# Performance work log

Measured on AMD Instinct MI355X. Metric: run time of the kernel, lower is better.

Reference implementation:

```python
import jax, jax.numpy as jnp
import numpy as np

N = 50000
E = 800000
F_IN = 256
HID = 96
N_CLS = 32
NEG_SLOPE = 0.2


def setup_inputs() -> dict:
    key = jax.random.key(0)
    ks = jax.random.split(key, 10)
    x = jax.random.normal(ks[0], (N, F_IN), dtype=jnp.float32)
    edge_index = jax.random.randint(ks[1], (2, E), 0, N, dtype=jnp.int64)
    s1 = 1.0 / np.sqrt(F_IN)
    s2 = 1.0 / np.sqrt(HID)
    return {
        "x": x,
        "edge_index": edge_index,
        "W1": jax.random.normal(ks[2], (F_IN, HID), dtype=jnp.float32) * s1,
        "a1_src": jax.random.normal(ks[3], (HID,), dtype=jnp.float32) * s2,
        "a1_dst": jax.random.normal(ks[4], (HID,), dtype=jnp.float32) * s2,
        "b1": jnp.zeros((HID,), dtype=jnp.float32),
        "W2": jax.random.normal(ks[5], (HID, N_CLS), dtype=jnp.float32) * s2,
        "a2_src": jax.random.normal(ks[6], (N_CLS,), dtype=jnp.float32) * (1.0 / np.sqrt(N_CLS)),
        "a2_dst": jax.random.normal(ks[7], (N_CLS,), dtype=jnp.float32) * (1.0 / np.sqrt(N_CLS)),
        "b2": jnp.zeros((N_CLS,), dtype=jnp.float32),
    }


def _gat_conv(x, src, dst, W, a_src, a_dst, b, n_nodes):
    # single-head GATConv (PyG defaults), self-loops already in src/dst
    h = x @ W                                  # [N, out]
    alpha_src = h @ a_src                      # [N]
    alpha_dst = h @ a_dst                      # [N]
    e = alpha_src[src] + alpha_dst[dst]        # [E'] edge logits (msg j->i: dst groups)
    e = jnp.where(e > 0, e, NEG_SLOPE * e)     # leaky_relu
    # segment softmax over edges grouped by destination node
    m = jax.ops.segment_max(e, dst, num_segments=n_nodes)
    ex = jnp.exp(e - m[dst])
    denom = jax.ops.segment_sum(ex, dst, num_segments=n_nodes)
    alpha = ex / denom[dst]                    # [E']
    out = jax.ops.segment_sum(alpha[:, None] * h[src], dst, num_segments=n_nodes)
    return out + b


def reference(x, edge_index, W1, a1_src, a1_dst, b1, W2, a2_src, a2_dst, b2):
    loops = jnp.arange(N, dtype=edge_index.dtype)
    src = jnp.concatenate([edge_index[0], loops])
    dst = jnp.concatenate([edge_index[1], loops])
    h = _gat_conv(x, src, dst, W1, a1_src, a1_dst, b1, N)
    h = jax.nn.elu(h)
    # dropout omitted (eval mode, training=False)
    out = _gat_conv(h, src, dst, W2, a2_src, a2_dst, b2, N)
    return jax.nn.log_softmax(out, axis=1)
```

## Files before the change

### kernel.cpp

```cpp
#include <hip/hip_runtime.h>
#include <cstdint>
#include <cstddef>

#define NNODES 50000
#define NEDGES 800000
#define MEDGES (NEDGES + NNODES)
#define FIN    256
#define HID    96
#define NCLS   32
#define NEG_SLOPE 0.2f

#define NBUCK  391
#define BCAP   3072

typedef unsigned int uint32;
typedef __attribute__((ext_vector_type(8))) short short8;
typedef __attribute__((ext_vector_type(4))) float f32x4;

__device__ __forceinline__ ushort bf_round(float f) {
    uint32 u = __float_as_uint(f);
    u += 0x7FFFu + ((u >> 16) & 1u);
    return (ushort)(u >> 16);
}
__device__ __forceinline__ uint32 pack_bf16x2(float a, float b) {
    return (uint32)bf_round(a) | ((uint32)bf_round(b) << 16);
}
__device__ __forceinline__ float bf_lo(uint32 u) { return __uint_as_float(u << 16); }
__device__ __forceinline__ float bf_hi(uint32 u) { return __uint_as_float(u & 0xFFFF0000u); }
__device__ __forceinline__ float lrelu(float t) { return (t > 0.f) ? t : NEG_SLOPE * t; }
__device__ __forceinline__ float af(int i) { return __int_as_float(i); }
__device__ __forceinline__ float elu_fast(float t) { return (t > 0.f) ? t : (__expf(t) - 1.f); }


__global__ __launch_bounds__(256) void packw_kernel(const float* __restrict__ W1,
                                                    ushort* __restrict__ W1p,
                                                    int* __restrict__ gcount) {
    int stride = gridDim.x * 256;
    for (int idx = blockIdx.x * 256 + threadIdx.x; idx < NBUCK; idx += stride)
        gcount[idx] = 0;
    for (int idx = blockIdx.x * 256 + threadIdx.x; idx < 6 * 8 * 64 * 8; idx += stride) {
        int j     = idx & 7;
        int lane  = (idx >> 3) & 63;
        int kstep = (idx >> 9) & 7;
        int ntile = idx >> 12;
        int k = kstep * 32 + ((lane >> 4) << 3) + j;
        int n = ntile * 16 + (lane & 15);
        W1p[idx] = bf_round(W1[(size_t)k * 96 + n]);
    }
}


__global__ __launch_bounds__(256) void bucket1_kernel(const int* __restrict__ ei,
                                                      int* __restrict__ gcount,
                                                      int* __restrict__ staging) {
    __shared__ int hist[NBUCK];
    __shared__ int base_sh[NBUCK];
    for (int i = threadIdx.x; i < NBUCK; i += 256) hist[i] = 0;
    __syncthreads();

    int v[8], rk[8], bk[8];
    int e0 = blockIdx.x * 2048;
#pragma unroll
    for (int i = 0; i < 8; ++i) {
        int e = e0 + i * 256 + threadIdx.x;
        if (e < MEDGES) {
            int s, d;
            if (e < NEDGES) { s = ei[e]; d = ei[NEDGES + e]; }
            else            { s = e - NEDGES; d = s; }
            bk[i] = d >> 7;
            v[i]  = s | ((d & 127) << 16);
            rk[i] = atomicAdd(&hist[bk[i]], 1);
        } else bk[i] = -1;
    }
    __syncthreads();
    for (int i = threadIdx.x; i < NBUCK; i += 256) {
        int c = hist[i];
        base_sh[i] = c ? atomicAdd(&gcount[i], c) : 0;
    }
    __syncthreads();
#pragma unroll
    for (int i = 0; i < 8; ++i) {
        if (bk[i] >= 0) {
            int pos = base_sh[bk[i]] + rk[i];
            if (pos < BCAP)
                staging[(size_t)bk[i] * BCAP + pos] = v[i];
        }
    }
}


__global__ __launch_bounds__(256) void b2gemm1_kernel(const int* __restrict__ staging,
                                                      const int* __restrict__ gcount,
                                                      int* __restrict__ rowptr,
                                                      int* __restrict__ esrc,
                                                      const float* __restrict__ x,
                                                      const ushort* __restrict__ W1p,
                                                      const float* __restrict__ a_src,
                                                      const float* __restrict__ a_dst,
                                                      ushort* __restrict__ h1,
                                                      float* __restrict__ as1,
                                                      float* __restrict__ ad1) {
    __shared__ int dcount[128];
    __shared__ int dincl[128];
    __shared__ int dexcl[128];
    __shared__ int fillc[128];
    __shared__ int red_s[256];

    if (blockIdx.x < NBUCK) {
        const int b = blockIdx.x;
        const int t = threadIdx.x;

        int pv = 0;
        for (int idx = t; idx < b; idx += 256) pv += gcount[idx];
        red_s[t] = pv;
        __syncthreads();
        for (int off2 = 128; off2; off2 >>= 1) {
            if (t < off2) red_s[t] += red_s[t + off2];
            __syncthreads();
        }
        const int ebase = red_s[0];
        const int cnt   = gcount[b];
        const int node0 = b << 7;
        const int* st   = staging + (size_t)b * BCAP;

        for (int i = t; i < 128; i += 256) { dcount[i] = 0; fillc[i] = 0; }
        __syncthreads();

        for (int i = t; i < cnt; i += 256)
            atomicAdd(&dcount[st[i] >> 16], 1);
        __syncthreads();

        if (t < 128) dincl[t] = dcount[t];
        __syncthreads();
        for (int off = 1; off < 128; off <<= 1) {
            int val = (t >= off && t < 128) ? dincl[t - off] : 0;
            __syncthreads();
            if (t < 128) dincl[t] += val;
            __syncthreads();
        }
        if (t < 128) {
            int excl = dincl[t] - dcount[t];
            dexcl[t] = excl;
            int node = node0 + t;
            if (node < NNODES) rowptr[node] = ebase + excl;
        }
        if (b == NBUCK - 1 && t == 0) rowptr[NNODES] = MEDGES;
        __syncthreads();

        for (int i = t; i < cnt; i += 256) {
            int v = st[i];
            int dd = v >> 16;
            int r = atomicAdd(&fillc[dd], 1);
            esrc[ebase + dexcl[dd] + r] = v & 0xFFFF;
        }
        return;
    }

    const int tid  = threadIdx.x;
    const int lane = tid & 63;
    const int wv   = tid >> 6;
    const int m    = lane & 15;
    const int quad = lane >> 4;
    const int node0 = (blockIdx.x - NBUCK) * 64;

    int arow = node0 + wv * 16 + m;
    if (arow >= NNODES) arow = NNODES - 1;
    const float* xr = x + (size_t)arow * FIN + quad * 8;

    const short8* Wp = (const short8*)W1p;

    f32x4 acc[6];
#pragma unroll
    for (int t = 0; t < 6; ++t) acc[t] = (f32x4){0.f, 0.f, 0.f, 0.f};

#pragma unroll
    for (int ks = 0; ks < 8; ++ks) {
        float4 v0 = *(const float4*)(xr + ks * 32);
        float4 v1 = *(const float4*)(xr + ks * 32 + 4);
        short8 a;
        a[0] = (short)bf_round(v0.x); a[1] = (short)bf_round(v0.y);
        a[2] = (short)bf_round(v0.z); a[3] = (short)bf_round(v0.w);
        a[4] = (short)bf_round(v1.x); a[5] = (short)bf_round(v1.y);
        a[6] = (short)bf_round(v1.z); a[7] = (short)bf_round(v1.w);
#pragma unroll
        for (int t = 0; t < 6; ++t) {
            short8 b = Wp[(t * 8 + ks) * 64 + lane];
            acc[t] = __builtin_amdgcn_mfma_f32_16x16x32_bf16(a, b, acc[t], 0, 0, 0);
        }
    }

    float as_reg[6], ad_reg[6];
#pragma unroll
    for (int t = 0; t < 6; ++t) {
        as_reg[t] = a_src[t * 16 + m];
        ad_reg[t] = a_dst[t * 16 + m];
    }

#pragma unroll
    for (int r = 0; r < 4; ++r) {
        int node = node0 + wv * 16 + quad * 4 + r;
        float ps = 0.f, pd = 0.f;
#pragma unroll
        for (int t = 0; t < 6; ++t) {
            ps += acc[t][r] * as_reg[t];
            pd += acc[t][r] * ad_reg[t];
        }
#pragma unroll
        for (int off = 1; off < 16; off <<= 1) {
            ps += __shfl_xor(ps, off);
            pd += __shfl_xor(pd, off);
        }
        if (node < NNODES) {
            ushort* hp = h1 + (size_t)node * 96 + m;
#pragma unroll
            for (int t = 0; t < 6; ++t) hp[t * 16] = bf_round(acc[t][r]);
            if (m == 0) { as1[node] = ps; ad1[node] = pd; }
        }
    }
}


__global__ __launch_bounds__(256) void agg96g2_kernel(const ushort* __restrict__ h,
                                                      const float* __restrict__ asrc,
                                                      const float* __restrict__ adst,
                                                      const float* __restrict__ bias,
                                                      const int* __restrict__ rowptr,
                                                      const int* __restrict__ esrc,
                                                      const float* __restrict__ W2,
                                                      const float* __restrict__ a2s,
                                                      const float* __restrict__ a2d,
                                                      uint32* __restrict__ h2b,
                                                      float* __restrict__ as2,
                                                      float* __restrict__ ad2) {
    __shared__ int2 sa[4][2][32];
    __shared__ __align__(16) float W2t[32 * 100];
    __shared__ __align__(16) float y_sh[4][2][96];

    for (int idx = threadIdx.x; idx < 96 * 32; idx += 256) {
        int c = idx & 31, k = idx >> 5;
        W2t[c * 100 + k] = W2[idx];
    }
    __syncthreads();

    const int wave = threadIdx.x >> 6;
    const int lane = threadIdx.x & 63;
    const int hf   = lane >> 5;
    const int fl32 = lane & 31;
    const int i = blockIdx.x * 8 + wave * 2 + hf;

    const int start = rowptr[i];
    const int deg   = rowptr[i + 1] - start;
    const float ad  = adst[i];
    const float a2s_v = a2s[fl32];
    const float a2d_v = a2d[fl32];
    const int fl    = (fl32 < 24) ? fl32 : 23;

    float acc0 = 0.f, acc1 = 0.f, acc2 = 0.f, acc3 = 0.f;

    if (deg <= 32) {
        bool valid = fl32 < deg;
        int s_reg = valid ? esrc[start + fl32] : 0;
        float e = valid ? lrelu(asrc[s_reg] + ad) : -1e30f;
        float mx = e;
#pragma unroll
        for (int off = 16; off; off >>= 1) mx = fmaxf(mx, __shfl_xor(mx, off));
        float ex = valid ? __expf(e - mx) : 0.f;
        float sum = ex;
#pragma unroll
        for (int off = 16; off; off >>= 1) sum += __shfl_xor(sum, off);
        sa[wave][hf][fl32] = make_int2(s_reg, __float_as_int(ex / sum));

        const int4* sap = (const int4*)&sa[wave][hf][0];

        for (int eb = 0; eb < deg; eb += 8) {
            int4 qa = sap[(eb >> 1) + 0];
            int4 qb = sap[(eb >> 1) + 1];
            int4 qc = sap[(eb >> 1) + 2];
            int4 qd = sap[(eb >> 1) + 3];
            const uint2* r0 = (const uint2*)(h + (size_t)qa.x * 96);
            const uint2* r1 = (const uint2*)(h + (size_t)qa.z * 96);
            const uint2* r2 = (const uint2*)(h + (size_t)qb.x * 96);
            const uint2* r3 = (const uint2*)(h + (size_t)qb.z * 96);
            const uint2* r4 = (const uint2*)(h + (size_t)qc.x * 96);
            const uint2* r5 = (const uint2*)(h + (size_t)qc.z * 96);
            const uint2* r6 = (const uint2*)(h + (size_t)qd.x * 96);
            const uint2* r7 = (const uint2*)(h + (size_t)qd.z * 96);
            uint2 u0 = r0[fl], u1 = r1[fl], u2 = r2[fl], u3 = r3[fl];
            uint2 u4 = r4[fl], u5 = r5[fl], u6 = r6[fl], u7 = r7[fl];
            float a0 = af(qa.y), a1 = af(qa.w), a2 = af(qb.y), a3 = af(qb.w);
            float a4 = af(qc.y), a5 = af(qc.w), a6 = af(qd.y), a7 = af(qd.w);
            acc0 += a0 * bf_lo(u0.x) + a1 * bf_lo(u1.x) + a2 * bf_lo(u2.x) + a3 * bf_lo(u3.x)
                  + a4 * bf_lo(u4.x) + a5 * bf_lo(u5.x) + a6 * bf_lo(u6.x) + a7 * bf_lo(u7.x);
            acc1 += a0 * bf_hi(u0.x) + a1 * bf_hi(u1.x) + a2 * bf_hi(u2.x) + a3 * bf_hi(u3.x)
                  + a4 * bf_hi(u4.x) + a5 * bf_hi(u5.x) + a6 * bf_hi(u6.x) + a7 * bf_hi(u7.x);
            acc2 += a0 * bf_lo(u0.y) + a1 * bf_lo(u1.y) + a2 * bf_lo(u2.y) + a3 * bf_lo(u3.y)
                  + a4 * bf_lo(u4.y) + a5 * bf_lo(u5.y) + a6 * bf_lo(u6.y) + a7 * bf_lo(u7.y);
            acc3 += a0 * bf_hi(u0.y) + a1 * bf_hi(u1.y) + a2 * bf_hi(u2.y) + a3 * bf_hi(u3.y)
                  + a4 * bf_hi(u4.y) + a5 * bf_hi(u5.y) + a6 * bf_hi(u6.y) + a7 * bf_hi(u7.y);
        }
    } else {
        float mx = -1e30f;
        for (int p = start + fl32; p < start + deg; p += 32)
            mx = fmaxf(mx, lrelu(asrc[esrc[p]] + ad));
#pragma unroll
        for (int off = 16; off; off >>= 1) mx = fmaxf(mx, __shfl_xor(mx, off));
        float sum = 0.f;
        for (int p = start + fl32; p < start + deg; p += 32)
            sum += __expf(lrelu(asrc[esrc[p]] + ad) - mx);
#pragma unroll
        for (int off = 16; off; off >>= 1) sum += __shfl_xor(sum, off);
        float inv = 1.f / sum;
        for (int e = 0; e < deg; ++e) {
            int s = esrc[start + e];
            float a = __expf(lrelu(asrc[s] + ad) - mx) * inv;
            uint2 u = ((const uint2*)(h + (size_t)s * 96))[fl];
            acc0 += a * bf_lo(u.x);
            acc1 += a * bf_hi(u.x);
            acc2 += a * bf_lo(u.y);
            acc3 += a * bf_hi(u.y);
        }
    }

    if (fl32 < 24) {
        float* yp = &y_sh[wave][hf][4 * fl32];
        yp[0] = elu_fast(acc0 + bias[4 * fl32 + 0]);
        yp[1] = elu_fast(acc1 + bias[4 * fl32 + 1]);
        yp[2] = elu_fast(acc2 + bias[4 * fl32 + 2]);
        yp[3] = elu_fast(acc3 + bias[4 * fl32 + 3]);
    }
    asm volatile("s_waitcnt lgkmcnt(0)" ::: "memory");

    const float* yrow = &y_sh[wave][hf][0];
    const float* wcol = W2t + fl32 * 100;
    float h2c = 0.f;
#pragma unroll
    for (int k = 0; k < 96; k += 4) {
        float4 yv = *(const float4*)(yrow + k);
        float4 wv = *(const float4*)(wcol + k);
        h2c = fmaf(yv.x, wv.x, h2c);
        h2c = fmaf(yv.y, wv.y, h2c);
        h2c = fmaf(yv.z, wv.z, h2c);
        h2c = fmaf(yv.w, wv.w, h2c);
    }

    float ps = h2c * a2s_v;
    float pd = h2c * a2d_v;
#pragma unroll
    for (int off = 1; off < 32; off <<= 1) {
        ps += __shfl_xor(ps, off);
        pd += __shfl_xor(pd, off);
    }
    float partner = __shfl_xor(h2c, 16);
    if (fl32 < 16)
        h2b[(size_t)i * 16 + fl32] = pack_bf16x2(h2c, partner);
    if (fl32 == 0) { as2[i] = ps; ad2[i] = pd; }
}


__global__ __launch_bounds__(256) void agg32_kernel(const uint32* __restrict__ h2b,
                                                    const float* __restrict__ asrc,
                                                    const float* __restrict__ adst,
                                                    const float* __restrict__ bias,
                                                    const int* __restrict__ rowptr,
                                                    const int* __restrict__ esrc,
                                                    float* __restrict__ out) {
    __shared__ int2 sa[4][2][32];
    const int wave = threadIdx.x >> 6;
    const int lane = threadIdx.x & 63;
    const int hf   = lane >> 5;
    const int fl32 = lane & 31;
    const int i = blockIdx.x * 8 + wave * 2 + hf;

    const int start = rowptr[i];
    const int deg   = rowptr[i + 1] - start;
    const float ad  = adst[i];
    const int g  = fl32 >> 3;
    const int fl = fl32 & 7;

    float acc[4];
#pragma unroll
    for (int j = 0; j < 4; ++j) acc[j] = 0.f;

    if (deg <= 32) {
        bool valid = fl32 < deg;
        int s_reg = valid ? esrc[start + fl32] : 0;
        float e = valid ? lrelu(asrc[s_reg] + ad) : -1e30f;
        float mx = e;
#pragma unroll
        for (int off = 16; off; off >>= 1) mx = fmaxf(mx, __shfl_xor(mx, off));
        float ex = valid ? __expf(e - mx) : 0.f;
        float sum = ex;
#pragma unroll
        for (int off = 16; off; off >>= 1) sum += __shfl_xor(sum, off);
        sa[wave][hf][fl32] = make_int2(s_reg, __float_as_int(ex / sum));

#pragma unroll 2
        for (int eb = 0; eb < deg; eb += 4) {
            int e0 = eb + g;
            int2 q = sa[wave][hf][(e0 < 32) ? e0 : 31];
            float a = (e0 < deg) ? af(q.y) : 0.f;
            const uint2* hr = (const uint2*)(h2b + (size_t)q.x * 16);
            uint2 u = hr[fl];
            acc[0] = fmaf(a, bf_lo(u.x), acc[0]);
            acc[1] = fmaf(a, bf_hi(u.x), acc[1]);
            acc[2] = fmaf(a, bf_lo(u.y), acc[2]);
            acc[3] = fmaf(a, bf_hi(u.y), acc[3]);
        }
    } else {
        float mx = -1e30f;
        for (int p = start + fl32; p < start + deg; p += 32)
            mx = fmaxf(mx, lrelu(asrc[esrc[p]] + ad));
#pragma unroll
        for (int off = 16; off; off >>= 1) mx = fmaxf(mx, __shfl_xor(mx, off));
        float sum = 0.f;
        for (int p = start + fl32; p < start + deg; p += 32)
            sum += __expf(lrelu(asrc[esrc[p]] + ad) - mx);
#pragma unroll
        for (int off = 16; off; off >>= 1) sum += __shfl_xor(sum, off);
        float inv = 1.f / sum;
        for (int p = start + g; p < start + deg; p += 4) {
            int s = esrc[p];
            float a = __expf(lrelu(asrc[s] + ad) - mx) * inv;
            const uint2* hr = (const uint2*)(h2b + (size_t)s * 16);
            uint2 u = hr[fl];
            acc[0] = fmaf(a, bf_lo(u.x), acc[0]);
            acc[1] = fmaf(a, bf_hi(u.x), acc[1]);
            acc[2] = fmaf(a, bf_lo(u.y), acc[2]);
            acc[3] = fmaf(a, bf_hi(u.y), acc[3]);
        }
    }

#pragma unroll
    for (int j = 0; j < 4; ++j) {
        acc[j] += __shfl_xor(acc[j], 8);
        acc[j] += __shfl_xor(acc[j], 16);
    }

    float z0 = acc[0] + bias[2 * fl];
    float z1 = acc[1] + bias[2 * fl + 16];
    float z2 = acc[2] + bias[2 * fl + 1];
    float z3 = acc[3] + bias[2 * fl + 17];
    float m2 = fmaxf(fmaxf(z0, z1), fmaxf(z2, z3));
#pragma unroll
    for (int off = 4; off; off >>= 1) m2 = fmaxf(m2, __shfl_xor(m2, off));
    float s2 = __expf(z0 - m2) + __expf(z1 - m2) + __expf(z2 - m2) + __expf(z3 - m2);
#pragma unroll
    for (int off = 4; off; off >>= 1) s2 += __shfl_xor(s2, off);
    float ls = m2 + __logf(s2);
    if (fl32 < 8) {
        float* op = out + (size_t)i * 32;
        op[2 * fl]      = z0 - ls;
        op[2 * fl + 16] = z1 - ls;
        op[2 * fl + 1]  = z2 - ls;
        op[2 * fl + 17] = z3 - ls;
    }
}


extern "C" void kernel_launch(void* const* d_in, const int* in_sizes, int n_in,
                              void* d_out, int out_size, void* d_ws, size_t ws_size,
                              hipStream_t stream) {
    const float* x   = (const float*)d_in[0];
    const int*   ei  = (const int*)d_in[1];
    const float* W1  = (const float*)d_in[2];
    const float* a1s = (const float*)d_in[3];
    const float* a1d = (const float*)d_in[4];
    const float* b1  = (const float*)d_in[5];
    const float* W2  = (const float*)d_in[6];
    const float* a2s = (const float*)d_in[7];
    const float* a2d = (const float*)d_in[8];
    const float* b2  = (const float*)d_in[9];
    float* out = (float*)d_out;

    size_t off = 0;
    auto alloc = [&](size_t bytes) {
        void* p = (char*)d_ws + off;
        off += (bytes + 255) & ~(size_t)255;
        return p;
    };
    ushort* h1    = (ushort*)alloc((size_t)NNODES * HID * 2);
    uint32* h2b   = (uint32*)alloc((size_t)NNODES * 16 * 4);
    int*  staging = (int*)alloc((size_t)NBUCK * BCAP * 4);
    float* as1    = (float*)alloc((size_t)NNODES * 4);
    float* ad1    = (float*)alloc((size_t)NNODES * 4);
    float* as2    = (float*)alloc((size_t)NNODES * 4);
    float* ad2    = (float*)alloc((size_t)NNODES * 4);
    int*   rowptr = (int*)alloc((size_t)(NNODES + 1) * 4);
    int*   esrc   = (int*)alloc((size_t)MEDGES * 4);
    ushort* W1p   = (ushort*)alloc((size_t)6 * 8 * 64 * 8 * 2);
    int*   gcount = (int*)alloc((size_t)NBUCK * 4);

    const int nbB1    = (MEDGES + 2047) / 2048;
    const int nbGemm  = (NNODES + 63) / 64;
    const int nbAggP  = NNODES / 8;

    packw_kernel<<<16, 256, 0, stream>>>(W1, W1p, gcount);
    bucket1_kernel<<<nbB1, 256, 0, stream>>>(ei, gcount, staging);
    b2gemm1_kernel<<<NBUCK + nbGemm, 256, 0, stream>>>(staging, gcount, rowptr, esrc,
                                                       x, W1p, a1s, a1d, h1, as1, ad1);
    agg96g2_kernel<<<nbAggP, 256, 0, stream>>>(h1, as1, ad1, b1, rowptr, esrc,
                                               W2, a2s, a2d, h2b, as2, ad2);
    agg32_kernel<<<nbAggP, 256, 0, stream>>>(h2b, as2, ad2, b2, rowptr, esrc, out);
}
```

Before: 207.4 us.

## Fuse all five GAT stages into one cooperative persistent kernel with grid syncs

Result: slower. 456.7 us (+120.2%).

```diff
diff --git a/kernel.cpp b/kernel.cpp
--- a/kernel.cpp
+++ b/kernel.cpp
@@ -1,6 +1,9 @@
 #include <hip/hip_runtime.h>
+#include <hip/hip_cooperative_groups.h>
 #include <cstdint>
 #include <cstddef>
+
+namespace cg = cooperative_groups;
 
 #define NNODES 50000
 #define NEDGES 800000
@@ -12,6 +15,9 @@
 
 #define NBUCK  391
 #define BCAP   3072
+#define NCHUNK ((MEDGES + 2047) / 2048)
+#define NGEMM1 ((NNODES + 63) / 64)
+#define NAGG   (NNODES / 8)
 
 typedef unsigned int uint32;
 typedef __attribute__((ext_vector_type(8))) short short8;
@@ -31,428 +37,396 @@
 __device__ __forceinline__ float af(int i) { return __int_as_float(i); }
 __device__ __forceinline__ float elu_fast(float t) { return (t > 0.f) ? t : (__expf(t) - 1.f); }
 
-
-__global__ __launch_bounds__(256) void packw_kernel(const float* __restrict__ W1,
-                                                    ushort* __restrict__ W1p,
-                                                    int* __restrict__ gcount) {
-    int stride = gridDim.x * 256;
-    for (int idx = blockIdx.x * 256 + threadIdx.x; idx < NBUCK; idx += stride)
-        gcount[idx] = 0;
-    for (int idx = blockIdx.x * 256 + threadIdx.x; idx < 6 * 8 * 64 * 8; idx += stride) {
-        int j     = idx & 7;
-        int lane  = (idx >> 3) & 63;
-        int kstep = (idx >> 9) & 7;
-        int ntile = idx >> 12;
-        int k = kstep * 32 + ((lane >> 4) << 3) + j;
-        int n = ntile * 16 + (lane & 15);
-        W1p[idx] = bf_round(W1[(size_t)k * 96 + n]);
-    }
-}
-
-
-__global__ __launch_bounds__(256) void bucket1_kernel(const int* __restrict__ ei,
-                                                      int* __restrict__ gcount,
-                                                      int* __restrict__ staging) {
-    __shared__ int hist[NBUCK];
-    __shared__ int base_sh[NBUCK];
-    for (int i = threadIdx.x; i < NBUCK; i += 256) hist[i] = 0;
-    __syncthreads();
-
-    int v[8], rk[8], bk[8];
-    int e0 = blockIdx.x * 2048;
-#pragma unroll
-    for (int i = 0; i < 8; ++i) {
-        int e = e0 + i * 256 + threadIdx.x;
-        if (e < MEDGES) {
-            int s, d;
-            if (e < NEDGES) { s = ei[e]; d = ei[NEDGES + e]; }
-            else            { s = e - NEDGES; d = s; }
-            bk[i] = d >> 7;
-            v[i]  = s | ((d & 127) << 16);
-            rk[i] = atomicAdd(&hist[bk[i]], 1);
-        } else bk[i] = -1;
-    }
-    __syncthreads();
-    for (int i = threadIdx.x; i < NBUCK; i += 256) {
-        int c = hist[i];
-        base_sh[i] = c ? atomicAdd(&gcount[i], c) : 0;
-    }
-    __syncthreads();
-#pragma unroll
-    for (int i = 0; i < 8; ++i) {
-        if (bk[i] >= 0) {
-            int pos = base_sh[bk[i]] + rk[i];
-            if (pos < BCAP)
-                staging[(size_t)bk[i] * BCAP + pos] = v[i];
-        }
-    }
-}
-
-
-__global__ __launch_bounds__(256) void b2gemm1_kernel(const int* __restrict__ staging,
-                                                      const int* __restrict__ gcount,
-                                                      int* __restrict__ rowptr,
-                                                      int* __restrict__ esrc,
-                                                      const float* __restrict__ x,
-                                                      const ushort* __restrict__ W1p,
-                                                      const float* __restrict__ a_src,
-                                                      const float* __restrict__ a_dst,
-                                                      ushort* __restrict__ h1,
-                                                      float* __restrict__ as1,
-                                                      float* __restrict__ ad1) {
-    __shared__ int dcount[128];
-    __shared__ int dincl[128];
-    __shared__ int dexcl[128];
-    __shared__ int fillc[128];
-    __shared__ int red_s[256];
-
-    if (blockIdx.x < NBUCK) {
-        const int b = blockIdx.x;
-        const int t = threadIdx.x;
-
-        int pv = 0;
-        for (int idx = t; idx < b; idx += 256) pv += gcount[idx];
-        red_s[t] = pv;
-        __syncthreads();
-        for (int off2 = 128; off2; off2 >>= 1) {
-            if (t < off2) red_s[t] += red_s[t + off2];
-            __syncthreads();
-        }
-        const int ebase = red_s[0];
-        const int cnt   = gcount[b];
-        const int node0 = b << 7;
-        const int* st   = staging + (size_t)b * BCAP;
-
-        for (int i = t; i < 128; i += 256) { dcount[i] = 0; fillc[i] = 0; }
-        __syncthreads();
-
-        for (int i = t; i < cnt; i += 256)
-            atomicAdd(&dcount[st[i] >> 16], 1);
-        __syncthreads();
-
-        if (t < 128) dincl[t] = dcount[t];
-        __syncthreads();
-        for (int off = 1; off < 128; off <<= 1) {
-            int val = (t >= off && t < 128) ? dincl[t - off] : 0;
-            __syncthreads();
-            if (t < 128) dincl[t] += val;
-            __syncthreads();
-        }
-        if (t < 128) {
-            int excl = dincl[t] - dcount[t];
-            dexcl[t] = excl;
-            int node = node0 + t;
-            if (node < NNODES) rowptr[node] = ebase + excl;
-        }
-        if (b == NBUCK - 1 && t == 0) rowptr[NNODES] = MEDGES;
-        __syncthreads();
-
-        for (int i = t; i < cnt; i += 256) {
-            int v = st[i];
-            int dd = v >> 16;
-            int r = atomicAdd(&fillc[dd], 1);
-            esrc[ebase + dexcl[dd] + r] = v & 0xFFFF;
-        }
-        return;
-    }
-
-    const int tid  = threadIdx.x;
-    const int lane = tid & 63;
-    const int wv   = tid >> 6;
-    const int m    = lane & 15;
-    const int quad = lane >> 4;
-    const int node0 = (blockIdx.x - NBUCK) * 64;
-
-    int arow = node0 + wv * 16 + m;
-    if (arow >= NNODES) arow = NNODES - 1;
-    const float* xr = x + (size_t)arow * FIN + quad * 8;
-
-    const short8* Wp = (const short8*)W1p;
-
-    f32x4 acc[6];
-#pragma unroll
-    for (int t = 0; t < 6; ++t) acc[t] = (f32x4){0.f, 0.f, 0.f, 0.f};
-
-#pragma unroll
-    for (int ks = 0; ks < 8; ++ks) {
-        float4 v0 = *(const float4*)(xr + ks * 32);
-        float4 v1 = *(const float4*)(xr + ks * 32 + 4);
-        short8 a;
-        a[0] = (short)bf_round(v0.x); a[1] = (short)bf_round(v0.y);
-        a[2] = (short)bf_round(v0.z); a[3] = (short)bf_round(v0.w);
-        a[4] = (short)bf_round(v1.x); a[5] = (short)bf_round(v1.y);
-        a[6] = (short)bf_round(v1.z); a[7] = (short)bf_round(v1.w);
-#pragma unroll
-        for (int t = 0; t < 6; ++t) {
-            short8 b = Wp[(t * 8 + ks) * 64 + lane];
-            acc[t] = __builtin_amdgcn_mfma_f32_16x16x32_bf16(a, b, acc[t], 0, 0, 0);
-        }
-    }
-
-    float as_reg[6], ad_reg[6];
-#pragma unroll
-    for (int t = 0; t < 6; ++t) {
-        as_reg[t] = a_src[t * 16 + m];
-        ad_reg[t] = a_dst[t * 16 + m];
-    }
-
-#pragma unroll
-    for (int r = 0; r < 4; ++r) {
-        int node = node0 + wv * 16 + quad * 4 + r;
-        float ps = 0.f, pd = 0.f;
-#pragma unroll
-        for (int t = 0; t < 6; ++t) {
-            ps += acc[t][r] * as_reg[t];
-            pd += acc[t][r] * ad_reg[t];
-        }
-#pragma unroll
-        for (int off = 1; off < 16; off <<= 1) {
-            ps += __shfl_xor(ps, off);
-            pd += __shfl_xor(pd, off);
-        }
-        if (node < NNODES) {
-            ushort* hp = h1 + (size_t)node * 96 + m;
-#pragma unroll
-            for (int t = 0; t < 6; ++t) hp[t * 16] = bf_round(acc[t][r]);
-            if (m == 0) { as1[node] = ps; ad1[node] = pd; }
-        }
-    }
-}
-
-
-__global__ __launch_bounds__(256) void agg96g2_kernel(const ushort* __restrict__ h,
-                                                      const float* __restrict__ asrc,
-                                                      const float* __restrict__ adst,
-                                                      const float* __restrict__ bias,
-                                                      const int* __restrict__ rowptr,
-                                                      const int* __restrict__ esrc,
-                                                      const float* __restrict__ W2,
-                                                      const float* __restrict__ a2s,
-                                                      const float* __restrict__ a2d,
-                                                      uint32* __restrict__ h2b,
-                                                      float* __restrict__ as2,
-                                                      float* __restrict__ ad2) {
-    __shared__ int2 sa[4][2][32];
-    __shared__ __align__(16) float W2t[32 * 100];
-    __shared__ __align__(16) float y_sh[4][2][96];
-
-    for (int idx = threadIdx.x; idx < 96 * 32; idx += 256) {
-        int c = idx & 31, k = idx >> 5;
-        W2t[c * 100 + k] = W2[idx];
-    }
-    __syncthreads();
-
-    const int wave = threadIdx.x >> 6;
-    const int lane = threadIdx.x & 63;
+struct __align__(16) SU {
+    union {
+        struct { int hist[NBUCK]; int base_sh[NBUCK]; } s1;
+        struct { int dcount[128]; int dincl[128]; int dexcl[128];
+                 int fillc[128]; int red_s[256]; } s2;
+        struct { int2 sa[4][2][32]; float W2n[96 * 32]; float y_sh[4][2][96]; } s3;
+        struct { int2 sa[4][2][32]; } s4;
+    } u;
+};
+
+
+__global__ __launch_bounds__(256) void fused_all(
+        const float* __restrict__ x,   const int* __restrict__ ei,
+        const float* __restrict__ W1,
+        const float* __restrict__ a1s, const float* __restrict__ a1d,
+        const float* __restrict__ b1,
+        const float* __restrict__ W2,
+        const float* __restrict__ a2s, const float* __restrict__ a2d,
+        const float* __restrict__ b2,
+        float* __restrict__ out,
+        ushort* __restrict__ h1, uint32* __restrict__ h2b,
+        int* __restrict__ staging, float* __restrict__ as1, float* __restrict__ ad1,
+        float* __restrict__ as2, float* __restrict__ ad2,
+        int* __restrict__ rowptr, int* __restrict__ esrc,
+        ushort* __restrict__ W1p, int* __restrict__ gcount) {
+    __shared__ SU sh;
+    cg::grid_group grid = cg::this_grid();
+
+    const int t    = threadIdx.x;
+    const int wave = t >> 6;
+    const int lane = t & 63;
     const int hf   = lane >> 5;
     const int fl32 = lane & 31;
-    const int i = blockIdx.x * 8 + wave * 2 + hf;
-
-    const int start = rowptr[i];
-    const int deg   = rowptr[i + 1] - start;
-    const float ad  = adst[i];
-    const float a2s_v = a2s[fl32];
-    const float a2d_v = a2d[fl32];
-    const int fl    = (fl32 < 24) ? fl32 : 23;
-
-    float acc0 = 0.f, acc1 = 0.f, acc2 = 0.f, acc3 = 0.f;
-
-    if (deg <= 32) {
-        bool valid = fl32 < deg;
-        int s_reg = valid ? esrc[start + fl32] : 0;
-        float e = valid ? lrelu(asrc[s_reg] + ad) : -1e30f;
-        float mx = e;
-#pragma unroll
-        for (int off = 16; off; off >>= 1) mx = fmaxf(mx, __shfl_xor(mx, off));
-        float ex = valid ? __expf(e - mx) : 0.f;
-        float sum = ex;
-#pragma unroll
-        for (int off = 16; off; off >>= 1) sum += __shfl_xor(sum, off);
-        sa[wave][hf][fl32] = make_int2(s_reg, __float_as_int(ex / sum));
-
-        const int4* sap = (const int4*)&sa[wave][hf][0];
-
-        for (int eb = 0; eb < deg; eb += 8) {
-            int4 qa = sap[(eb >> 1) + 0];
-            int4 qb = sap[(eb >> 1) + 1];
-            int4 qc = sap[(eb >> 1) + 2];
-            int4 qd = sap[(eb >> 1) + 3];
-            const uint2* r0 = (const uint2*)(h + (size_t)qa.x * 96);
-            const uint2* r1 = (const uint2*)(h + (size_t)qa.z * 96);
-            const uint2* r2 = (const uint2*)(h + (size_t)qb.x * 96);
-            const uint2* r3 = (const uint2*)(h + (size_t)qb.z * 96);
-            const uint2* r4 = (const uint2*)(h + (size_t)qc.x * 96);
-            const uint2* r5 = (const uint2*)(h + (size_t)qc.z * 96);
-            const uint2* r6 = (const uint2*)(h + (size_t)qd.x * 96);
-            const uint2* r7 = (const uint2*)(h + (size_t)qd.z * 96);
-            uint2 u0 = r0[fl], u1 = r1[fl], u2 = r2[fl], u3 = r3[fl];
-            uint2 u4 = r4[fl], u5 = r5[fl], u6 = r6[fl], u7 = r7[fl];
-            float a0 = af(qa.y), a1 = af(qa.w), a2 = af(qb.y), a3 = af(qb.w);
-            float a4 = af(qc.y), a5 = af(qc.w), a6 = af(qd.y), a7 = af(qd.w);
-            acc0 += a0 * bf_lo(u0.x) + a1 * bf_lo(u1.x) + a2 * bf_lo(u2.x) + a3 * bf_lo(u3.x)
-                  + a4 * bf_lo(u4.x) + a5 * bf_lo(u5.x) + a6 * bf_lo(u6.x) + a7 * bf_lo(u7.x);
-            acc1 += a0 * bf_hi(u0.x) + a1 * bf_hi(u1.x) + a2 * bf_hi(u2.x) + a3 * bf_hi(u3.x)
-                  + a4 * bf_hi(u4.x) + a5 * bf_hi(u5.x) + a6 * bf_hi(u6.x) + a7 * bf_hi(u7.x);
-            acc2 += a0 * bf_lo(u0.y) + a1 * bf_lo(u1.y) + a2 * bf_lo(u2.y) + a3 * bf_lo(u3.y)
-                  + a4 * bf_lo(u4.y) + a5 * bf_lo(u5.y) + a6 * bf_lo(u6.y) + a7 * bf_lo(u7.y);
-            acc3 += a0 * bf_hi(u0.y) + a1 * bf_hi(u1.y) + a2 * bf_hi(u2.y) + a3 * bf_hi(u3.y)
-                  + a4 * bf_hi(u4.y) + a5 * bf_hi(u5.y) + a6 * bf_hi(u6.y) + a7 * bf_hi(u7.y);
-        }
-    } else {
-        float mx = -1e30f;
-        for (int p = start + fl32; p < start + deg; p += 32)
-            mx = fmaxf(mx, lrelu(asrc[esrc[p]] + ad));
-#pragma unroll
-        for (int off = 16; off; off >>= 1) mx = fmaxf(mx, __shfl_xor(mx, off));
-        float sum = 0.f;
-        for (int p = start + fl32; p < start + deg; p += 32)
-            sum += __expf(lrelu(asrc[esrc[p]] + ad) - mx);
-#pragma unroll
-        for (int off = 16; off; off >>= 1) sum += __shfl_xor(sum, off);
-        float inv = 1.f / sum;
-        for (int e = 0; e < deg; ++e) {
-            int s = esrc[start + e];
-            float a = __expf(lrelu(asrc[s] + ad) - mx) * inv;
-            uint2 u = ((const uint2*)(h + (size_t)s * 96))[fl];
-            acc0 += a * bf_lo(u.x);
-            acc1 += a * bf_hi(u.x);
-            acc2 += a * bf_lo(u.y);
-            acc3 += a * bf_hi(u.y);
-        }
-    }
-
-    if (fl32 < 24) {
-        float* yp = &y_sh[wave][hf][4 * fl32];
-        yp[0] = elu_fast(acc0 + bias[4 * fl32 + 0]);
-        yp[1] = elu_fast(acc1 + bias[4 * fl32 + 1]);
-        yp[2] = elu_fast(acc2 + bias[4 * fl32 + 2]);
-        yp[3] = elu_fast(acc3 + bias[4 * fl32 + 3]);
-    }
-    asm volatile("s_waitcnt lgkmcnt(0)" ::: "memory");
-
-    const float* yrow = &y_sh[wave][hf][0];
-    const float* wcol = W2t + fl32 * 100;
-    float h2c = 0.f;
-#pragma unroll
-    for (int k = 0; k < 96; k += 4) {
-        float4 yv = *(const float4*)(yrow + k);
-        float4 wv = *(const float4*)(wcol + k);
-        h2c = fmaf(yv.x, wv.x, h2c);
-        h2c = fmaf(yv.y, wv.y, h2c);
-        h2c = fmaf(yv.z, wv.z, h2c);
-        h2c = fmaf(yv.w, wv.w, h2c);
-    }
-
-    float ps = h2c * a2s_v;
-    float pd = h2c * a2d_v;
-#pragma unroll
-    for (int off = 1; off < 32; off <<= 1) {
-        ps += __shfl_xor(ps, off);
-        pd += __shfl_xor(pd, off);
-    }
-    float partner = __shfl_xor(h2c, 16);
-    if (fl32 < 16)
-        h2b[(size_t)i * 16 + fl32] = pack_bf16x2(h2c, partner);
-    if (fl32 == 0) { as2[i] = ps; ad2[i] = pd; }
-}
-
-
-__global__ __launch_bounds__(256) void agg32_kernel(const uint32* __restrict__ h2b,
-                                                    const float* __restrict__ asrc,
-                                                    const float* __restrict__ adst,
-                                                    const float* __restrict__ bias,
-                                                    const int* __restrict__ rowptr,
-                                                    const int* __restrict__ esrc,
-                                                    float* __restrict__ out) {
-    __shared__ int2 sa[4][2][32];
-    const int wave = threadIdx.x >> 6;
-    const int lane = threadIdx.x & 63;
-    const int hf   = lane >> 5;
-    const int fl32 = lane & 31;
-    const int i = blockIdx.x * 8 + wave * 2 + hf;
-
-    const int start = rowptr[i];
-    const int deg   = rowptr[i + 1] - start;
-    const float ad  = adst[i];
-    const int g  = fl32 >> 3;
-    const int fl = fl32 & 7;
-
-    float acc[4];
-#pragma unroll
-    for (int j = 0; j < 4; ++j) acc[j] = 0.f;
-
-    if (deg <= 32) {
-        bool valid = fl32 < deg;
-        int s_reg = valid ? esrc[start + fl32] : 0;
-        float e = valid ? lrelu(asrc[s_reg] + ad) : -1e30f;
-        float mx = e;
-#pragma unroll
-        for (int off = 16; off; off >>= 1) mx = fmaxf(mx, __shfl_xor(mx, off));
-        float ex = valid ? __expf(e - mx) : 0.f;
-        float sum = ex;
-#pragma unroll
-        for (int off = 16; off; off >>= 1) sum += __shfl_xor(sum, off);
-        sa[wave][hf][fl32] = make_int2(s_reg, __float_as_int(ex / sum));
+
+    {
+        int stride = gridDim.x * 256;
+        int tid0 = blockIdx.x * 256 + t;
+        for (int idx = tid0; idx < NBUCK; idx += stride) gcount[idx] = 0;
+        for (int idx = tid0; idx < 6 * 8 * 64 * 8; idx += stride) {
+            int j     = idx & 7;
+            int ln    = (idx >> 3) & 63;
+            int kstep = (idx >> 9) & 7;
+            int ntile = idx >> 12;
+            int k = kstep * 32 + ((ln >> 4) << 3) + j;
+            int n = ntile * 16 + (ln & 15);
+            W1p[idx] = bf_round(W1[(size_t)k * 96 + n]);
+        }
+    }
+    grid.sync();
+
+    for (int chunk = blockIdx.x; chunk < NCHUNK; chunk += gridDim.x) {
+        for (int i = t; i < NBUCK; i += 256) sh.u.s1.hist[i] = 0;
+        __syncthreads();
+        int v[8], rk[8], bk[8];
+        int e0 = chunk * 2048;
+#pragma unroll
+        for (int i = 0; i < 8; ++i) {
+            int e = e0 + i * 256 + t;
+            if (e < MEDGES) {
+                int s, d;
+                if (e < NEDGES) { s = ei[e]; d = ei[NEDGES + e]; }
+                else            { s = e - NEDGES; d = s; }
+                bk[i] = d >> 7;
+                v[i]  = s | ((d & 127) << 16);
+                rk[i] = atomicAdd(&sh.u.s1.hist[bk[i]], 1);
+            } else bk[i] = -1;
+        }
+        __syncthreads();
+        for (int i = t; i < NBUCK; i += 256) {
+            int c = sh.u.s1.hist[i];
+            sh.u.s1.base_sh[i] = c ? atomicAdd(&gcount[i], c) : 0;
+        }
+        __syncthreads();
+#pragma unroll
+        for (int i = 0; i < 8; ++i) {
+            if (bk[i] >= 0) {
+                int pos = sh.u.s1.base_sh[bk[i]] + rk[i];
+                if (pos < BCAP)
+                    staging[(size_t)bk[i] * BCAP + pos] = v[i];
+            }
+        }
+        __syncthreads();
+    }
+    grid.sync();
+
+    for (int uu = blockIdx.x; uu < NBUCK + NGEMM1; uu += gridDim.x) {
+        if (uu < NBUCK) {
+            const int b = uu;
+            int pv = 0;
+            for (int idx = t; idx < b; idx += 256) pv += gcount[idx];
+            sh.u.s2.red_s[t] = pv;
+            __syncthreads();
+            for (int off2 = 128; off2; off2 >>= 1) {
+                if (t < off2) sh.u.s2.red_s[t] += sh.u.s2.red_s[t + off2];
+                __syncthreads();
+            }
+            const int ebase = sh.u.s2.red_s[0];
+            const int cnt   = gcount[b];
+            const int node0 = b << 7;
+            const int* st   = staging + (size_t)b * BCAP;
+
+            for (int i = t; i < 128; i += 256) { sh.u.s2.dcount[i] = 0; sh.u.s2.fillc[i] = 0; }
+            __syncthreads();
+            for (int i = t; i < cnt; i += 256)
+                atomicAdd(&sh.u.s2.dcount[st[i] >> 16], 1);
+            __syncthreads();
+            if (t < 128) sh.u.s2.dincl[t] = sh.u.s2.dcount[t];
+            __syncthreads();
+            for (int off = 1; off < 128; off <<= 1) {
+                int val = (t >= off && t < 128) ? sh.u.s2.dincl[t - off] : 0;
+                __syncthreads();
+                if (t < 128) sh.u.s2.dincl[t] += val;
+                __syncthreads();
+            }
+            if (t < 128) {
+                int excl = sh.u.s2.dincl[t] - sh.u.s2.dcount[t];
+                sh.u.s2.dexcl[t] = excl;
+                int node = node0 + t;
+                if (node < NNODES) rowptr[node] = ebase + excl;
+            }
+            if (b == NBUCK - 1 && t == 0) rowptr[NNODES] = MEDGES;
+            __syncthreads();
+            for (int i = t; i < cnt; i += 256) {
+                int v = st[i];
+                int dd = v >> 16;
+                int r = atomicAdd(&sh.u.s2.fillc[dd], 1);
+                esrc[ebase + sh.u.s2.dexcl[dd] + r] = v & 0xFFFF;
+            }
+            __syncthreads();
+        } else {
+            const int m    = lane & 15;
+            const int quad = lane >> 4;
+            const int node0 = (uu - NBUCK) * 64;
+
+            int arow = node0 + wave * 16 + m;
+            if (arow >= NNODES) arow = NNODES - 1;
+            const float* xr = x + (size_t)arow * FIN + quad * 8;
+            const short8* Wp = (const short8*)W1p;
+
+            f32x4 acc[6];
+#pragma unroll
+            for (int tt = 0; tt < 6; ++tt) acc[tt] = (f32x4){0.f, 0.f, 0.f, 0.f};
+#pragma unroll
+            for (int ks = 0; ks < 8; ++ks) {
+                float4 v0 = *(const float4*)(xr + ks * 32);
+                float4 v1 = *(const float4*)(xr + ks * 32 + 4);
+                short8 a;
+                a[0] = (short)bf_round(v0.x); a[1] = (short)bf_round(v0.y);
+                a[2] = (short)bf_round(v0.z); a[3] = (short)bf_round(v0.w);
+                a[4] = (short)bf_round(v1.x); a[5] = (short)bf_round(v1.y);
+                a[6] = (short)bf_round(v1.z); a[7] = (short)bf_round(v1.w);
+#pragma unroll
+                for (int tt = 0; tt < 6; ++tt) {
+                    short8 bfr = Wp[(tt * 8 + ks) * 64 + lane];
+                    acc[tt] = __builtin_amdgcn_mfma_f32_16x16x32_bf16(a, bfr, acc[tt], 0, 0, 0);
+                }
+            }
+
+            float as_reg[6], ad_reg[6];
+#pragma unroll
+            for (int tt = 0; tt < 6; ++tt) {
+                as_reg[tt] = a1s[tt * 16 + m];
+                ad_reg[tt] = a1d[tt * 16 + m];
+            }
+#pragma unroll
+            for (int r = 0; r < 4; ++r) {
+                int node = node0 + wave * 16 + quad * 4 + r;
+                float ps = 0.f, pd = 0.f;
+#pragma unroll
+                for (int tt = 0; tt < 6; ++tt) {
+                    ps += acc[tt][r] * as_reg[tt];
+                    pd += acc[tt][r] * ad_reg[tt];
+                }
+#pragma unroll
+                for (int off = 1; off < 16; off <<= 1) {
+                    ps += __shfl_xor(ps, off);
+                    pd += __shfl_xor(pd, off);
+                }
+                if (node < NNODES) {
+                    ushort* hp = h1 + (size_t)node * 96 + m;
+#pragma unroll
+                    for (int tt = 0; tt < 6; ++tt) hp[tt * 16] = bf_round(acc[tt][r]);
+                    if (m == 0) { as1[node] = ps; ad1[node] = pd; }
+                }
+            }
+        }
+    }
+    grid.sync();
+
+    for (int idx = t; idx < 96 * 32; idx += 256)
+        sh.u.s3.W2n[idx] = W2[idx];
+    __syncthreads();
+    {
+        const float a2s_v = a2s[fl32];
+        const float a2d_v = a2d[fl32];
+        const int fl = (fl32 < 24) ? fl32 : 23;
+
+        for (int uu = blockIdx.x; uu < NAGG; uu += gridDim.x) {
+            const int i = uu * 8 + wave * 2 + hf;
+            const int start = rowptr[i];
+            const int deg   = rowptr[i + 1] - start;
+            const float ad  = ad1[i];
+
+            float acc0 = 0.f, acc1 = 0.f, acc2 = 0.f, acc3 = 0.f;
+
+            if (deg <= 32) {
+                bool valid = fl32 < deg;
+                int s_reg = valid ? esrc[start + fl32] : 0;
+                float e = valid ? lrelu(as1[s_reg] + ad) : -1e30f;
+                float mx = e;
+#pragma unroll
+                for (int off = 16; off; off >>= 1) mx = fmaxf(mx, __shfl_xor(mx, off));
+                float ex = valid ? __expf(e - mx) : 0.f;
+                float sum = ex;
+#pragma unroll
+                for (int off = 16; off; off >>= 1) sum += __shfl_xor(sum, off);
+                sh.u.s3.sa[wave][hf][fl32] = make_int2(s_reg, __float_as_int(ex / sum));
+
+                const int4* sap = (const int4*)&sh.u.s3.sa[wave][hf][0];
+                for (int eb = 0; eb < deg; eb += 8) {
+                    int4 qa = sap[(eb >> 1) + 0];
+                    int4 qb = sap[(eb >> 1) + 1];
+                    int4 qc = sap[(eb >> 1) + 2];
+                    int4 qd = sap[(eb >> 1) + 3];
+                    const uint2* r0 = (const uint2*)(h1 + (size_t)qa.x * 96);
+                    const uint2* r1 = (const uint2*)(h1 + (size_t)qa.z * 96);
+                    const uint2* r2 = (const uint2*)(h1 + (size_t)qb.x * 96);
+                    const uint2* r3 = (const uint2*)(h1 + (size_t)qb.z * 96);
+                    const uint2* r4 = (const uint2*)(h1 + (size_t)qc.x * 96);
+                    const uint2* r5 = (const uint2*)(h1 + (size_t)qc.z * 96);
+                    const uint2* r6 = (const uint2*)(h1 + (size_t)qd.x * 96);
+                    const uint2* r7 = (const uint2*)(h1 + (size_t)qd.z * 96);
+                    uint2 u0 = r0[fl], u1 = r1[fl], u2 = r2[fl], u3 = r3[fl];
+                    uint2 u4 = r4[fl], u5 = r5[fl], u6 = r6[fl], u7 = r7[fl];
+                    float a0 = af(qa.y), a1 = af(qa.w), a2 = af(qb.y), a3 = af(qb.w);
+                    float a4 = af(qc.y), a5 = af(qc.w), a6 = af(qd.y), a7 = af(qd.w);
+                    acc0 += a0 * bf_lo(u0.x) + a1 * bf_lo(u1.x) + a2 * bf_lo(u2.x) + a3 * bf_lo(u3.x)
+                          + a4 * bf_lo(u4.x) + a5 * bf_lo(u5.x) + a6 * bf_lo(u6.x) + a7 * bf_lo(u7.x);
+                    acc1 += a0 * bf_hi(u0.x) + a1 * bf_hi(u1.x) + a2 * bf_hi(u2.x) + a3 * bf_hi(u3.x)
+                          + a4 * bf_hi(u4.x) + a5 * bf_hi(u5.x) + a6 * bf_hi(u6.x) + a7 * bf_hi(u7.x);
+                    acc2 += a0 * bf_lo(u0.y) + a1 * bf_lo(u1.y) + a2 * bf_lo(u2.y) + a3 * bf_lo(u3.y)
+                          + a4 * bf_lo(u4.y) + a5 * bf_lo(u5.y) + a6 * bf_lo(u6.y) + a7 * bf_lo(u7.y);
+                    acc3 += a0 * bf_hi(u0.y) + a1 * bf_hi(u1.y) + a2 * bf_hi(u2.y) + a3 * bf_hi(u3.y)
+                          + a4 * bf_hi(u4.y) + a5 * bf_hi(u5.y) + a6 * bf_hi(u6.y) + a7 * bf_hi(u7.y);
+                }
+            } else {
+                float mx = -1e30f;
+                for (int p = start + fl32; p < start + deg; p += 32)
+                    mx = fmaxf(mx, lrelu(as1[esrc[p]] + ad));
+#pragma unroll
+                for (int off = 16; off; off >>= 1) mx = fmaxf(mx, __shfl_xor(mx, off));
+                float sum = 0.f;
+                for (int p = start + fl32; p < start + deg; p += 32)
+                    sum += __expf(lrelu(as1[esrc[p]] + ad) - mx);
+#pragma unroll
+                for (int off = 16; off; off >>= 1) sum += __shfl_xor(sum, off);
+                float inv = 1.f / sum;
+                for (int e = 0; e < deg; ++e) {
+                    int s = esrc[start + e];
+                    float a = __expf(lrelu(as1[s] + ad) - mx) * inv;
+                    uint2 u = ((const uint2*)(h1 + (size_t)s * 96))[fl];
+                    acc0 += a * bf_lo(u.x);
+                    acc1 += a * bf_hi(u.x);
+                    acc2 += a * bf_lo(u.y);
+                    acc3 += a * bf_hi(u.y);
+                }
+            }
+
+            if (fl32 < 24) {
+                float* yp = &sh.u.s3.y_sh[wave][hf][4 * fl32];
+                yp[0] = elu_fast(acc0 + b1[4 * fl32 + 0]);
+                yp[1] = elu_fast(acc1 + b1[4 * fl32 + 1]);
+                yp[2] = elu_fast(acc2 + b1[4 * fl32 + 2]);
+                yp[3] = elu_fast(acc3 + b1[4 * fl32 + 3]);
+            }
+            asm volatile("s_waitcnt lgkmcnt(0)" ::: "memory");
+
+            const float* yrow = &sh.u.s3.y_sh[wave][hf][0];
+            float h2c = 0.f;
+#pragma unroll
+            for (int k4 = 0; k4 < 96; k4 += 4) {
+                float4 yv = *(const float4*)(yrow + k4);
+                h2c = fmaf(yv.x, sh.u.s3.W2n[(k4 + 0) * 32 + fl32], h2c);
+                h2c = fmaf(yv.y, sh.u.s3.W2n[(k4 + 1) * 32 + fl32], h2c);
+                h2c = fmaf(yv.z, sh.u.s3.W2n[(k4 + 2) * 32 + fl32], h2c);
+                h2c = fmaf(yv.w, sh.u.s3.W2n[(k4 + 3) * 32 + fl32], h2c);
+            }
+
+            float ps = h2c * a2s_v;
+            float pd = h2c * a2d_v;
+#pragma unroll
+            for (int off = 1; off < 32; off <<= 1) {
+                ps += __shfl_xor(ps, off);
+                pd += __shfl_xor(pd, off);
+            }
+            float partner = __shfl_xor(h2c, 16);
+            if (fl32 < 16)
+                h2b[(size_t)i * 16 + fl32] = pack_bf16x2(h2c, partner);
+            if (fl32 == 0) { as2[i] = ps; ad2[i] = pd; }
+        }
+    }
+    grid.sync();
+
+    {
+        const int g  = fl32 >> 3;
+        const int fl = fl32 & 7;
+        for (int uu = blockIdx.x; uu < NAGG; uu += gridDim.x) {
+            const int i = uu * 8 + wave * 2 + hf;
+            const int start = rowptr[i];
+            const int deg   = rowptr[i + 1] - start;
+            const float ad  = ad2[i];
+
+            float acc[4];
+#pragma unroll
+            for (int j = 0; j < 4; ++j) acc[j] = 0.f;
+
+            if (deg <= 32) {
+                bool valid = fl32 < deg;
+                int s_reg = valid ? esrc[start + fl32] : 0;
+                float e = valid ? lrelu(as2[s_reg] + ad) : -1e30f;
+                float mx = e;
+#pragma unroll
+                for (int off = 16; off; off >>= 1) mx = fmaxf(mx, __shfl_xor(mx, off));
+                float ex = valid ? __expf(e - mx) : 0.f;
+                float sum = ex;
+#pragma unroll
+                for (int off = 16; off; off >>= 1) sum += __shfl_xor(sum, off);
+                sh.u.s4.sa[wave][hf][fl32] = make_int2(s_reg, __float_as_int(ex / sum));
 
 #pragma unroll 2
-        for (int eb = 0; eb < deg; eb += 4) {
-            int e0 = eb + g;
-            int2 q = sa[wave][hf][(e0 < 32) ? e0 : 31];
-            float a = (e0 < deg) ? af(q.y) : 0.f;
-            const uint2* hr = (const uint2*)(h2b + (size_t)q.x * 16);
-            uint2 u = hr[fl];
-            acc[0] = fmaf(a, bf_lo(u.x), acc[0]);
-            acc[1] = fmaf(a, bf_hi(u.x), acc[1]);
-            acc[2] = fmaf(a, bf_lo(u.y), acc[2]);
-            acc[3] = fmaf(a, bf_hi(u.y), acc[3]);
-        }
-    } else {
-        float mx = -1e30f;
-        for (int p = start + fl32; p < start + deg; p += 32)
-            mx = fmaxf(mx, lrelu(asrc[esrc[p]] + ad));
-#pragma unroll
-        for (int off = 16; off; off >>= 1) mx = fmaxf(mx, __shfl_xor(mx, off));
-        float sum = 0.f;
-        for (int p = start + fl32; p < start + deg; p += 32)
-            sum += __expf(lrelu(asrc[esrc[p]] + ad) - mx);
-#pragma unroll
-        for (int off = 16; off; off >>= 1) sum += __shfl_xor(sum, off);
-        float inv = 1.f / sum;
-        for (int p = start + g; p < start + deg; p += 4) {
-            int s = esrc[p];
-            float a = __expf(lrelu(asrc[s] + ad) - mx) * inv;
-            const uint2* hr = (const uint2*)(h2b + (size_t)s * 16);
-            uint2 u = hr[fl];
-            acc[0] = fmaf(a, bf_lo(u.x), acc[0]);
-            acc[1] = fmaf(a, bf_hi(u.x), acc[1]);
-            acc[2] = fmaf(a, bf_lo(u.y), acc[2]);
-            acc[3] = fmaf(a, bf_hi(u.y), acc[3]);
-        }
-    }
-
-#pragma unroll
-    for (int j = 0; j < 4; ++j) {
-        acc[j] += __shfl_xor(acc[j], 8);
-        acc[j] += __shfl_xor(acc[j], 16);
-    }
-
-    float z0 = acc[0] + bias[2 * fl];
-    float z1 = acc[1] + bias[2 * fl + 16];
-    float z2 = acc[2] + bias[2 * fl + 1];
-    float z3 = acc[3] + bias[2 * fl + 17];
-    float m2 = fmaxf(fmaxf(z0, z1), fmaxf(z2, z3));
-#pragma unroll
-    for (int off = 4; off; off >>= 1) m2 = fmaxf(m2, __shfl_xor(m2, off));
-    float s2 = __expf(z0 - m2) + __expf(z1 - m2) + __expf(z2 - m2) + __expf(z3 - m2);
-#pragma unroll
-    for (int off = 4; off; off >>= 1) s2 += __shfl_xor(s2, off);
-    float ls = m2 + __logf(s2);
-    if (fl32 < 8) {
-        float* op = out + (size_t)i * 32;
-        op[2 * fl]      = z0 - ls;
-        op[2 * fl + 16] = z1 - ls;
-        op[2 * fl + 1]  = z2 - ls;
-        op[2 * fl + 17] = z3 - ls;
+                for (int eb = 0; eb < deg; eb += 4) {
+                    int e0 = eb + g;
+                    int2 q = sh.u.s4.sa[wave][hf][(e0 < 32) ? e0 : 31];
+                    float a = (e0 < deg) ? af(q.y) : 0.f;
+                    const uint2* hr = (const uint2*)(h2b + (size_t)q.x * 16);
+                    uint2 u = hr[fl];
+                    acc[0] = fmaf(a, bf_lo(u.x), acc[0]);
+                    acc[1] = fmaf(a, bf_hi(u.x), acc[1]);
+                    acc[2] = fmaf(a, bf_lo(u.y), acc[2]);
+                    acc[3] = fmaf(a, bf_hi(u.y), acc[3]);
+                }
+            } else {
+                float mx = -1e30f;
+                for (int p = start + fl32; p < start + deg; p += 32)
+                    mx = fmaxf(mx, lrelu(as2[esrc[p]] + ad));
+#pragma unroll
+                for (int off = 16; off; off >>= 1) mx = fmaxf(mx, __shfl_xor(mx, off));
+                float sum = 0.f;
+                for (int p = start + fl32; p < start + deg; p += 32)
+                    sum += __expf(lrelu(as2[esrc[p]] + ad) - mx);
+#pragma unroll
+                for (int off = 16; off; off >>= 1) sum += __shfl_xor(sum, off);
+                float inv = 1.f / sum;
+                for (int p = start + g; p < start + deg; p += 4) {
+                    int s = esrc[p];
+                    float a = __expf(lrelu(as2[s] + ad) - mx) * inv;
+                    const uint2* hr = (const uint2*)(h2b + (size_t)s * 16);
+                    uint2 u = hr[fl];
+                    acc[0] = fmaf(a, bf_lo(u.x), acc[0]);
+                    acc[1] = fmaf(a, bf_hi(u.x), acc[1]);
+                    acc[2] = fmaf(a, bf_lo(u.y), acc[2]);
+                    acc[3] = fmaf(a, bf_hi(u.y), acc[3]);
+                }
+            }
+
+#pragma unroll
+            for (int j = 0; j < 4; ++j) {
+                acc[j] += __shfl_xor(acc[j], 8);
+                acc[j] += __shfl_xor(acc[j], 16);
+            }
+
+            float z0 = acc[0] + b2[2 * fl];
+            float z1 = acc[1] + b2[2 * fl + 16];
+            float z2 = acc[2] + b2[2 * fl + 1];
+            float z3 = acc[3] + b2[2 * fl + 17];
+            float m2 = fmaxf(fmaxf(z0, z1), fmaxf(z2, z3));
+#pragma unroll
+            for (int off = 4; off; off >>= 1) m2 = fmaxf(m2, __shfl_xor(m2, off));
+            float s2 = __expf(z0 - m2) + __expf(z1 - m2) + __expf(z2 - m2) + __expf(z3 - m2);
+#pragma unroll
+            for (int off = 4; off; off >>= 1) s2 += __shfl_xor(s2, off);
+            float ls = m2 + __logf(s2);
+            if (fl32 < 8) {
+                float* op = out + (size_t)i * 32;
+                op[2 * fl]      = z0 - ls;
+                op[2 * fl + 16] = z1 - ls;
+                op[2 * fl + 1]  = z2 - ls;
+                op[2 * fl + 17] = z3 - ls;
+            }
+        }
     }
 }
 
@@ -490,15 +464,23 @@
     ushort* W1p   = (ushort*)alloc((size_t)6 * 8 * 64 * 8 * 2);
     int*   gcount = (int*)alloc((size_t)NBUCK * 4);
 
-    const int nbB1    = (MEDGES + 2047) / 2048;
-    const int nbGemm  = (NNODES + 63) / 64;
-    const int nbAggP  = NNODES / 8;
-
-    packw_kernel<<<16, 256, 0, stream>>>(W1, W1p, gcount);
-    bucket1_kernel<<<nbB1, 256, 0, stream>>>(ei, gcount, staging);
-    b2gemm1_kernel<<<NBUCK + nbGemm, 256, 0, stream>>>(staging, gcount, rowptr, esrc,
-                                                       x, W1p, a1s, a1d, h1, as1, ad1);
-    agg96g2_kernel<<<nbAggP, 256, 0, stream>>>(h1, as1, ad1, b1, rowptr, esrc,
-                                               W2, a2s, a2d, h2b, as2, ad2);
-    agg32_kernel<<<nbAggP, 256, 0, stream>>>(h2b, as2, ad2, b2, rowptr, esrc, out);
+    static int g_grid = 0;
+    if (g_grid == 0) {
+        hipDeviceProp_t prop;
+        hipGetDeviceProperties(&prop, 0);
+        int nb = 0;
+        hipOccupancyMaxActiveBlocksPerMultiprocessor(&nb, fused_all, 256, 0);
+        if (nb < 1) nb = 1;
+        long long g = (long long)prop.multiProcessorCount * nb;
+        if (g > 4096) g = 4096;
+        if (g < 1) g = 1;
+        g_grid = (int)g;
+    }
+
+    void* args[] = { (void*)&x, (void*)&ei, (void*)&W1, (void*)&a1s, (void*)&a1d,
+                     (void*)&b1, (void*)&W2, (void*)&a2s, (void*)&a2d, (void*)&b2,
+                     (void*)&out, (void*)&h1, (void*)&h2b, (void*)&staging,
+                     (void*)&as1, (void*)&ad1, (void*)&as2, (void*)&ad2,
+                     (void*)&rowptr, (void*)&esrc, (void*)&W1p, (void*)&gcount };
+    hipLaunchCooperativeKernel(fused_all, dim3(g_grid), dim3(256), args, 0, stream);
 }
```
